# Kernel optimization log

Measured on AMD Instinct MI355X. Metric: run time of the kernel, lower is better.

## Reference

```python
import jax, jax.numpy as jnp
import numpy as np

EMBED_DIM = 1024
NUM_HEADS = 16
HEAD_DIM = EMBED_DIM // NUM_HEADS


def setup_inputs() -> dict:
    key = jax.random.key(0)
    ks = jax.random.split(key, 9)
    B, S, E = 2, 2048, EMBED_DIM
    scale = 1.0 / np.sqrt(E)
    x = jax.random.normal(ks[0], (B, S, E), dtype=jnp.float32)
    Wq = jax.random.normal(ks[1], (E, E), dtype=jnp.float32) * scale
    bq = jax.random.normal(ks[2], (E,), dtype=jnp.float32) * 0.01
    Wk = jax.random.normal(ks[3], (E, E), dtype=jnp.float32) * scale
    bk = jax.random.normal(ks[4], (E,), dtype=jnp.float32) * 0.01
    Wv = jax.random.normal(ks[5], (E, E), dtype=jnp.float32) * scale
    bv = jax.random.normal(ks[6], (E,), dtype=jnp.float32) * 0.01
    Wo = jax.random.normal(ks[7], (E, E), dtype=jnp.float32) * scale
    bo = jax.random.normal(ks[8], (E,), dtype=jnp.float32) * 0.01
    return {"x": x, "Wq": Wq, "bq": bq, "Wk": Wk, "bk": bk,
            "Wv": Wv, "bv": bv, "Wo": Wo, "bo": bo}


def reference(x, Wq, bq, Wk, bk, Wv, bv, Wo, bo):
    B, S, E = x.shape
    H, D = NUM_HEADS, HEAD_DIM
    # projections (torch Linear: x @ W.T + b), reshape to (B, H, S, D)
    q = (x @ Wq.T + bq).reshape(B, S, H, D).transpose(0, 2, 1, 3)
    k = (x @ Wk.T + bk).reshape(B, S, H, D).transpose(0, 2, 1, 3)
    v = (x @ Wv.T + bv).reshape(B, S, H, D).transpose(0, 2, 1, 3)
    softmax_scale = 1.0 / np.sqrt(D)
    # (B, H, S, S) scores, causal mask, stable softmax
    scores = softmax_scale * jnp.einsum('bhsd,bhtd->bhst', q, k)
    causal = jnp.tril(jnp.ones((S, S), dtype=bool))  # True = keep
    scores = jnp.where(causal, scores, -jnp.inf)
    attn = jax.nn.softmax(scores, axis=-1)
    out = jnp.einsum('bhst,bhtd->bhsd', attn, v)  # (B, H, S, D)
    out = out.transpose(0, 2, 1, 3).reshape(B, S, E)
    return out @ Wo.T + bo
```

## Files before the change

### kernel.cpp

```cpp
#include <hip/hip_runtime.h>
#include <cstdint>
#include <cstddef>

#define SEQ   2048
#define BATCH 2
#define EMB   1024
#define NH    16
#define HD    64
#define MTOT  (BATCH * SEQ)
#define NX    (MTOT * EMB)
#define NW    (EMB * EMB)

typedef __bf16 bf16_t;
typedef __bf16 bf16x4 __attribute__((ext_vector_type(4)));
typedef __bf16 bf16x8 __attribute__((ext_vector_type(8)));
typedef float  f32x4  __attribute__((ext_vector_type(4)));
typedef float  f32x16 __attribute__((ext_vector_type(16)));

typedef __attribute__((address_space(1))) const void* as1cv;
typedef __attribute__((address_space(3))) void*       as3v;

__device__ __forceinline__ void async_cp16(const void* g, void* l) {
  __builtin_amdgcn_global_load_lds((as1cv)g, (as3v)l, 16, 0, 0);
}

__device__ __forceinline__ f32x4 mfma16(bf16x8 a, bf16x8 b, f32x4 c) {
  return __builtin_amdgcn_mfma_f32_16x16x32_bf16(a, b, c, 0, 0, 0);
}
__device__ __forceinline__ f32x16 mfma32(bf16x8 a, bf16x8 b, f32x16 c) {
  return __builtin_amdgcn_mfma_f32_32x32x16_bf16(a, b, c, 0, 0, 0);
}

__global__ __launch_bounds__(256) void cvt_all(
    const float* __restrict__ x,  const float* __restrict__ wq,
    const float* __restrict__ wk, const float* __restrict__ wv,
    const float* __restrict__ wo,
    bf16_t* __restrict__ xb,  bf16_t* __restrict__ wqb,
    bf16_t* __restrict__ wkb, bf16_t* __restrict__ wvb,
    bf16_t* __restrict__ wob) {
  long e = ((long)blockIdx.x * 256 + threadIdx.x) * 4;
  const float* s; bf16_t* d; long off;
  if (e < NX) { s = x; d = xb; off = e; }
  else {
    long e2 = e - NX;
    int w = (int)(e2 >> 20);
    off = e2 & (NW - 1);
    s = (w == 0) ? wq : (w == 1) ? wk : (w == 2) ? wv : wo;
    d = (w == 0) ? wqb : (w == 1) ? wkb : (w == 2) ? wvb : wob;
  }
  float4 v = *(const float4*)(s + off);
  bf16x4 o;
  o[0] = (bf16_t)v.x; o[1] = (bf16_t)v.y; o[2] = (bf16_t)v.z; o[3] = (bf16_t)v.w;
  *(bf16x4*)(d + off) = o;
}

__global__ __launch_bounds__(256) void vtrans(const bf16_t* __restrict__ V,
                                              bf16_t* __restrict__ VT) {
  const int hb = blockIdx.x;
  const int sb = blockIdx.y;
  const int h = hb & 15, b = hb >> 4;
  const int t = threadIdx.x;
  __shared__ __align__(16) bf16_t Ts[64 * 72];
  const bf16_t* Vp = V + ((size_t)(b * SEQ + sb * 64)) * EMB + h * HD;
  const int sr = t >> 4, d0 = (t & 15) * 4;
#pragma unroll
  for (int i = 0; i < 4; ++i) {
    bf16x4 v = *(const bf16x4*)(Vp + (size_t)(sr + 16 * i) * EMB + d0);
    *(bf16x4*)&Ts[(sr + 16 * i) * 72 + d0] = v;
  }
  __syncthreads();
  const int d = t >> 2, tc = (t & 3) * 16;
  __align__(16) bf16_t out[16];
#pragma unroll
  for (int j = 0; j < 16; ++j) out[j] = Ts[(tc + j) * 72 + d];
  bf16_t* dst = VT + ((size_t)hb * HD + d) * SEQ + sb * 64 + tc;
  *(uint4*)(dst)     = *(uint4*)&out[0];
  *(uint4*)(dst + 8) = *(uint4*)&out[8];
}

template <typename OT>
__global__ __launch_bounds__(256) void gemm_bt3(
    const bf16_t* __restrict__ A,
    const bf16_t* __restrict__ W0, const bf16_t* __restrict__ W1,
    const bf16_t* __restrict__ W2,
    const float* __restrict__ b0, const float* __restrict__ b1,
    const float* __restrict__ b2,
    OT* __restrict__ C0, OT* __restrict__ C1, OT* __restrict__ C2) {
  constexpr int K = EMB, N = EMB, BK = 64;
  const int z = blockIdx.z;
  const bf16_t* B    = (z == 0) ? W0 : (z == 1) ? W1 : W2;
  const float*  bias = (z == 0) ? b0 : (z == 1) ? b1 : b2;
  OT*           C    = (z == 0) ? C0 : (z == 1) ? C1 : C2;

  __shared__ __align__(16) bf16_t As[128 * BK];
  __shared__ __align__(16) bf16_t Bs[128 * BK];

  const int tid  = threadIdx.x;
  const int lane = tid & 63;
  const int wave = tid >> 6;
  const int quad = lane >> 4;
  const int l16  = lane & 15;
  const int wm   = (wave >> 1) * 64;
  const int wn   = (wave & 1) * 64;
  const int m0   = blockIdx.y * 128;
  const int n0   = blockIdx.x * 128;

  const int row0 = tid >> 3;
  const int slot = tid & 7;
  const bf16_t* gA[4];
  const bf16_t* gB[4];
#pragma unroll
  for (int i = 0; i < 4; ++i) {
    const int r    = row0 + 32 * i;
    const int scol = (slot ^ (r & 7)) * 8;
    gA[i] = A + (size_t)(m0 + r) * K + scol;
    gB[i] = B + (size_t)(n0 + r) * K + scol;
  }

  f32x4 acc[4][4] = {};
  const int sw = l16 & 7;

  for (int kk = 0; kk < K; kk += BK) {
#pragma unroll
    for (int i = 0; i < 4; ++i) {
      async_cp16(gA[i] + kk, &As[(tid + 256 * i) * 8]);
      async_cp16(gB[i] + kk, &Bs[(tid + 256 * i) * 8]);
    }
    __syncthreads();

    bf16x8 af[2][4], bfr[2][4];
#pragma unroll
    for (int ks = 0; ks < 2; ++ks) {
      const int cg = ks * 4 + quad;
      const int js = (cg ^ sw) * 8;
#pragma unroll
      for (int i = 0; i < 4; ++i) {
        af[ks][i]  = *(const bf16x8*)&As[(wm + i * 16 + l16) * BK + js];
        bfr[ks][i] = *(const bf16x8*)&Bs[(wn + i * 16 + l16) * BK + js];
      }
    }
#pragma unroll
    for (int ks = 0; ks < 2; ++ks)
#pragma unroll
      for (int i = 0; i < 4; ++i)
#pragma unroll
        for (int j = 0; j < 4; ++j)
          acc[i][j] = mfma16(af[ks][i], bfr[ks][j], acc[i][j]);
    __syncthreads();
  }

#pragma unroll
  for (int j = 0; j < 4; ++j) {
    const int col = n0 + wn + j * 16 + l16;
    const float bv = bias[col];
#pragma unroll
    for (int i = 0; i < 4; ++i) {
      const int row = m0 + wm + i * 16 + quad * 4;
#pragma unroll
      for (int r = 0; r < 4; ++r) {
        C[(size_t)(row + r) * N + col] = (OT)(acc[i][j][r] + bv);
      }
    }
  }
}

__global__ __launch_bounds__(256) void attn128(
    const bf16_t* __restrict__ Qg, const bf16_t* __restrict__ Kg,
    const bf16_t* __restrict__ VTg, bf16_t* __restrict__ Og) {
  const int hb  = blockIdx.x;
  const int y   = blockIdx.y;
  const int s   = (y < 8) ? (15 - y) : (y - 8);
  const int h   = hb & 15, b = hb >> 4;
  const int tid = threadIdx.x;
  const int lane = tid & 63, wave = tid >> 6;
  const int l31 = lane & 31, hi = lane >> 5;

  __shared__ __align__(16) bf16_t Ks[2][64 * 72];
  __shared__ __align__(16) bf16_t VsT[2][64 * 72];
  __shared__ __align__(16) bf16_t PQ[128 * 72];

  const size_t base = ((size_t)b * SEQ) * EMB + (size_t)h * HD;
  const bf16_t* Kp  = Kg + base;
  const bf16_t* VTp = VTg + (size_t)hb * HD * SEQ;

  const int kr0r = tid >> 3, kcol = (tid & 7) * 8;
  const int kr1r = kr0r + 32;
  const int lo0 = (tid >> 3) * 72 + kcol;
  const int lo1 = lo0 + 32 * 72;

  bf16_t* Pw = &PQ[wave * (32 * 72)];

  const int q0  = s * 128;
  const int nit = 2 * s + 2;
  const bf16_t* Qp = Qg + base + (size_t)q0 * EMB;

  uint4 kr0 = *(const uint4*)(Kp + (size_t)kr0r * EMB + kcol);
  uint4 kr1 = *(const uint4*)(Kp + (size_t)kr1r * EMB + kcol);
  uint4 vr0 = *(const uint4*)(VTp + (size_t)kr0r * SEQ + kcol);
  uint4 vr1 = *(const uint4*)(VTp + (size_t)kr1r * SEQ + kcol);

#pragma unroll
  for (int i = 0; i < 4; ++i) {
    const int c = tid + 256 * i;
    *(uint4*)&PQ[(c >> 3) * 72 + (c & 7) * 8] =
        *(const uint4*)(Qp + (size_t)(c >> 3) * EMB + (c & 7) * 8);
  }
  __syncthreads();

  bf16x8 qf[4];
#pragma unroll
  for (int kk = 0; kk < 4; ++kk)
    qf[kk] = *(const bf16x8*)&PQ[(32 * wave + l31) * 72 + kk * 16 + hi * 8];

  f32x16 acc_o0 = {}, acc_o1 = {};
  float l_i[16];
#pragma unroll
  for (int r = 0; r < 16; ++r) l_i[r] = 0.f;

  for (int it = 0; it < nit; ++it) {
    bf16_t* Kc = &Ks[it & 1][0];
    bf16_t* Vc = &VsT[it & 1][0];
    *(uint4*)&Kc[lo0] = kr0;
    *(uint4*)&Kc[lo1] = kr1;
    *(uint4*)&Vc[lo0] = vr0;
    *(uint4*)&Vc[lo1] = vr1;
    __syncthreads();

    if (it + 1 < nit) {
      const bf16_t* Kn  = Kp + (size_t)(it + 1) * 64 * EMB;
      const bf16_t* VTn = VTp + (it + 1) * 64;
      kr0 = *(const uint4*)(Kn + (size_t)kr0r * EMB + kcol);
      kr1 = *(const uint4*)(Kn + (size_t)kr1r * EMB + kcol);
      vr0 = *(const uint4*)(VTn + (size_t)kr0r * SEQ + kcol);
      vr1 = *(const uint4*)(VTn + (size_t)kr1r * SEQ + kcol);
    }

    const bool active = (64 * it <= q0 + 32 * wave + 31);
    if (active) {
      f32x16 acc0 = {}, acc1 = {};
#pragma unroll
      for (int kk = 0; kk < 4; ++kk) {
        const bf16x8 kf0 = *(const bf16x8*)&Kc[l31 * 72 + kk * 16 + hi * 8];
        const bf16x8 kf1 =
            *(const bf16x8*)&Kc[(32 + l31) * 72 + kk * 16 + hi * 8];
        acc0 = mfma32(qf[kk], kf0, acc0);
        acc1 = mfma32(qf[kk], kf1, acc1);
      }

      constexpr float SC2 = 0.18033688011112042f;
      if (it >= nit - 2) {
        const int row0 = q0 + 32 * wave + 4 * hi;
        const int c0 = 64 * it + l31, c1 = c0 + 32;
#pragma unroll
        for (int r = 0; r < 16; ++r) {
          const int row = row0 + (r & 3) + 8 * (r >> 2);
          float p0 = exp2f(__builtin_fmaf(acc0[r], SC2, -8.f));
          float p1 = exp2f(__builtin_fmaf(acc1[r], SC2, -8.f));
          if (c0 > row) p0 = 0.f;
          if (c1 > row) p1 = 0.f;
          l_i[r] += p0 + p1;
          const int rl = (r & 3) + 8 * (r >> 2) + 4 * hi;
          Pw[rl * 72 + l31]      = (bf16_t)p0;
          Pw[rl * 72 + 32 + l31] = (bf16_t)p1;
        }
      } else {
#pragma unroll
        for (int r = 0; r < 16; ++r) {
          const float p0 = exp2f(__builtin_fmaf(acc0[r], SC2, -8.f));
          const float p1 = exp2f(__builtin_fmaf(acc1[r], SC2, -8.f));
          l_i[r] += p0 + p1;
          const int rl = (r & 3) + 8 * (r >> 2) + 4 * hi;
          Pw[rl * 72 + l31]      = (bf16_t)p0;
          Pw[rl * 72 + 32 + l31] = (bf16_t)p1;
        }
      }

#pragma unroll
      for (int kk = 0; kk < 4; ++kk) {
        const bf16x8 pf = *(const bf16x8*)&Pw[l31 * 72 + kk * 16 + hi * 8];
        const bf16x8 vf0 = *(const bf16x8*)&Vc[l31 * 72 + kk * 16 + hi * 8];
        const bf16x8 vf1 =
            *(const bf16x8*)&Vc[(32 + l31) * 72 + kk * 16 + hi * 8];
        acc_o0 = mfma32(pf, vf0, acc_o0);
        acc_o1 = mfma32(pf, vf1, acc_o1);
      }
    }
  }

  bf16_t* Op = Og + base + (size_t)(q0 + 32 * wave) * EMB;
#pragma unroll
  for (int r = 0; r < 16; ++r) {
    float rs = l_i[r];
#pragma unroll
    for (int off = 1; off < 32; off <<= 1) rs += __shfl_xor(rs, off, 64);
    const float inv = 1.f / rs;
    const int rl = (r & 3) + 8 * (r >> 2) + 4 * hi;
    Op[(size_t)rl * EMB + l31]      = (bf16_t)(acc_o0[r] * inv);
    Op[(size_t)rl * EMB + 32 + l31] = (bf16_t)(acc_o1[r] * inv);
  }
}

extern "C" void kernel_launch(void* const* d_in, const int* in_sizes, int n_in,
                              void* d_out, int out_size, void* d_ws,
                              size_t ws_size, hipStream_t stream) {
  const float* x  = (const float*)d_in[0];
  const float* Wq = (const float*)d_in[1];
  const float* bq = (const float*)d_in[2];
  const float* Wk = (const float*)d_in[3];
  const float* bk = (const float*)d_in[4];
  const float* Wv = (const float*)d_in[5];
  const float* bv = (const float*)d_in[6];
  const float* Wo = (const float*)d_in[7];
  const float* bo = (const float*)d_in[8];
  float* out = (float*)d_out;

  char* p = (char*)d_ws;
  bf16_t* xb  = (bf16_t*)p; p += (size_t)NX * 2;
  bf16_t* wqb = (bf16_t*)p; p += (size_t)NW * 2;
  bf16_t* wkb = (bf16_t*)p; p += (size_t)NW * 2;
  bf16_t* wvb = (bf16_t*)p; p += (size_t)NW * 2;
  bf16_t* wob = (bf16_t*)p; p += (size_t)NW * 2;
  bf16_t* qb  = (bf16_t*)p; p += (size_t)NX * 2;
  bf16_t* kb  = (bf16_t*)p; p += (size_t)NX * 2;
  bf16_t* vb  = (bf16_t*)p; p += (size_t)NX * 2;
  bf16_t* ab  = (bf16_t*)p; p += (size_t)NX * 2;
  bf16_t* vtb = xb;

  const int ntot = NX + 4 * NW;
  cvt_all<<<dim3(ntot / 4 / 256), 256, 0, stream>>>(
      x, Wq, Wk, Wv, Wo, xb, wqb, wkb, wvb, wob);

  gemm_bt3<bf16_t><<<dim3(EMB / 128, MTOT / 128, 3), 256, 0, stream>>>(
      xb, wqb, wkb, wvb, bq, bk, bv, qb, kb, vb);

  vtrans<<<dim3(BATCH * NH, SEQ / 64), 256, 0, stream>>>(vb, vtb);

  attn128<<<dim3(BATCH * NH, SEQ / 128), 256, 0, stream>>>(qb, kb, vtb, ab);

  gemm_bt3<float><<<dim3(EMB / 128, MTOT / 128, 1), 256, 0, stream>>>(
      ab, wob, wob, wob, bo, bo, bo, out, out, out);
}
```

Baseline: 215.0 us.

## Keep attention probabilities in registers via transposed MFMA and shrink GEMM tile

The attention kernel now computes transposed scores (K·Qᵀ) so each lane holds one query row's probabilities. The P operand for the PV matmul is built in registers with cross-half shuffles instead of a round trip through shared memory, and the per-row sum needs a single shuffle. Output is staged through LDS for coalesced 16-byte stores, and launch bounds request 3 blocks per CU. The projection GEMMs switch from 128x128 to 128x64 tiles, doubling the grid for better CU fill at the cost of less operand reuse per block.

```diff
diff --git a/kernel.cpp b/kernel.cpp
--- a/kernel.cpp
+++ b/kernel.cpp
@@ -12,6 +12,7 @@
 #define NW    (EMB * EMB)
 
 typedef __bf16 bf16_t;
+typedef __bf16 bf16x2 __attribute__((ext_vector_type(2)));
 typedef __bf16 bf16x4 __attribute__((ext_vector_type(4)));
 typedef __bf16 bf16x8 __attribute__((ext_vector_type(8)));
 typedef float  f32x4  __attribute__((ext_vector_type(4)));
@@ -29,6 +30,16 @@
 }
 __device__ __forceinline__ f32x16 mfma32(bf16x8 a, bf16x8 b, f32x16 c) {
   return __builtin_amdgcn_mfma_f32_32x32x16_bf16(a, b, c, 0, 0, 0);
+}
+
+__device__ __forceinline__ uint32_t pk2(float a, float b) {
+  bf16x2 t; t[0] = (bf16_t)a; t[1] = (bf16_t)b;
+  return __builtin_bit_cast(uint32_t, t);
+}
+__device__ __forceinline__ bf16x8 mk_frag(uint32_t x, uint32_t y,
+                                          uint32_t z, uint32_t w) {
+  uint4 u; u.x = x; u.y = y; u.z = z; u.w = w;
+  return __builtin_bit_cast(bf16x8, u);
 }
 
 __global__ __launch_bounds__(256) void cvt_all(
@@ -93,56 +104,59 @@
   OT*           C    = (z == 0) ? C0 : (z == 1) ? C1 : C2;
 
   __shared__ __align__(16) bf16_t As[128 * BK];
-  __shared__ __align__(16) bf16_t Bs[128 * BK];
+  __shared__ __align__(16) bf16_t Bs[64 * BK];
 
   const int tid  = threadIdx.x;
   const int lane = tid & 63;
   const int wave = tid >> 6;
   const int quad = lane >> 4;
   const int l16  = lane & 15;
-  const int wm   = (wave >> 1) * 64;
-  const int wn   = (wave & 1) * 64;
+  const int wm   = wave * 32;
   const int m0   = blockIdx.y * 128;
-  const int n0   = blockIdx.x * 128;
+  const int n0   = blockIdx.x * 64;
 
   const int row0 = tid >> 3;
   const int slot = tid & 7;
   const bf16_t* gA[4];
-  const bf16_t* gB[4];
+  const bf16_t* gB[2];
 #pragma unroll
   for (int i = 0; i < 4; ++i) {
-    const int r    = row0 + 32 * i;
-    const int scol = (slot ^ (r & 7)) * 8;
-    gA[i] = A + (size_t)(m0 + r) * K + scol;
-    gB[i] = B + (size_t)(n0 + r) * K + scol;
-  }
-
-  f32x4 acc[4][4] = {};
+    const int r = row0 + 32 * i;
+    gA[i] = A + (size_t)(m0 + r) * K + (slot ^ (r & 7)) * 8;
+  }
+#pragma unroll
+  for (int i = 0; i < 2; ++i) {
+    const int r = row0 + 32 * i;
+    gB[i] = B + (size_t)(n0 + r) * K + (slot ^ (r & 7)) * 8;
+  }
+
+  f32x4 acc[2][4] = {};
   const int sw = l16 & 7;
 
   for (int kk = 0; kk < K; kk += BK) {
 #pragma unroll
-    for (int i = 0; i < 4; ++i) {
+    for (int i = 0; i < 4; ++i)
       async_cp16(gA[i] + kk, &As[(tid + 256 * i) * 8]);
+#pragma unroll
+    for (int i = 0; i < 2; ++i)
       async_cp16(gB[i] + kk, &Bs[(tid + 256 * i) * 8]);
-    }
     __syncthreads();
 
-    bf16x8 af[2][4], bfr[2][4];
+    bf16x8 af[2][2], bfr[2][4];
 #pragma unroll
     for (int ks = 0; ks < 2; ++ks) {
-      const int cg = ks * 4 + quad;
-      const int js = (cg ^ sw) * 8;
-#pragma unroll
-      for (int i = 0; i < 4; ++i) {
-        af[ks][i]  = *(const bf16x8*)&As[(wm + i * 16 + l16) * BK + js];
-        bfr[ks][i] = *(const bf16x8*)&Bs[(wn + i * 16 + l16) * BK + js];
-      }
+      const int js = ((ks * 4 + quad) ^ sw) * 8;
+#pragma unroll
+      for (int i = 0; i < 2; ++i)
+        af[ks][i] = *(const bf16x8*)&As[(wm + i * 16 + l16) * BK + js];
+#pragma unroll
+      for (int j = 0; j < 4; ++j)
+        bfr[ks][j] = *(const bf16x8*)&Bs[(j * 16 + l16) * BK + js];
     }
 #pragma unroll
     for (int ks = 0; ks < 2; ++ks)
 #pragma unroll
-      for (int i = 0; i < 4; ++i)
+      for (int i = 0; i < 2; ++i)
 #pragma unroll
         for (int j = 0; j < 4; ++j)
           acc[i][j] = mfma16(af[ks][i], bfr[ks][j], acc[i][j]);
@@ -151,10 +165,10 @@
 
 #pragma unroll
   for (int j = 0; j < 4; ++j) {
-    const int col = n0 + wn + j * 16 + l16;
+    const int col = n0 + j * 16 + l16;
     const float bv = bias[col];
 #pragma unroll
-    for (int i = 0; i < 4; ++i) {
+    for (int i = 0; i < 2; ++i) {
       const int row = m0 + wm + i * 16 + quad * 4;
 #pragma unroll
       for (int r = 0; r < 4; ++r) {
@@ -164,7 +178,7 @@
   }
 }
 
-__global__ __launch_bounds__(256) void attn128(
+__global__ __launch_bounds__(256, 3) void attn128(
     const bf16_t* __restrict__ Qg, const bf16_t* __restrict__ Kg,
     const bf16_t* __restrict__ VTg, bf16_t* __restrict__ Og) {
   const int hb  = blockIdx.x;
@@ -174,10 +188,11 @@
   const int tid = threadIdx.x;
   const int lane = tid & 63, wave = tid >> 6;
   const int l31 = lane & 31, hi = lane >> 5;
+  const bool h0 = (hi == 0);
 
   __shared__ __align__(16) bf16_t Ks[2][64 * 72];
   __shared__ __align__(16) bf16_t VsT[2][64 * 72];
-  __shared__ __align__(16) bf16_t PQ[128 * 72];
+  __shared__ __align__(16) bf16_t Qs[128 * 64];
 
   const size_t base = ((size_t)b * SEQ) * EMB + (size_t)h * HD;
   const bf16_t* Kp  = Kg + base;
@@ -185,10 +200,8 @@
 
   const int kr0r = tid >> 3, kcol = (tid & 7) * 8;
   const int kr1r = kr0r + 32;
-  const int lo0 = (tid >> 3) * 72 + kcol;
+  const int lo0 = kr0r * 72 + kcol;
   const int lo1 = lo0 + 32 * 72;
-
-  bf16_t* Pw = &PQ[wave * (32 * 72)];
 
   const int q0  = s * 128;
   const int nit = 2 * s + 2;
@@ -202,7 +215,7 @@
 #pragma unroll
   for (int i = 0; i < 4; ++i) {
     const int c = tid + 256 * i;
-    *(uint4*)&PQ[(c >> 3) * 72 + (c & 7) * 8] =
+    *(uint4*)&Qs[(c >> 3) * 64 + (c & 7) * 8] =
         *(const uint4*)(Qp + (size_t)(c >> 3) * EMB + (c & 7) * 8);
   }
   __syncthreads();
@@ -210,12 +223,10 @@
   bf16x8 qf[4];
 #pragma unroll
   for (int kk = 0; kk < 4; ++kk)
-    qf[kk] = *(const bf16x8*)&PQ[(32 * wave + l31) * 72 + kk * 16 + hi * 8];
-
-  f32x16 acc_o0 = {}, acc_o1 = {};
-  float l_i[16];
-#pragma unroll
-  for (int r = 0; r < 16; ++r) l_i[r] = 0.f;
+    qf[kk] = *(const bf16x8*)&Qs[(32 * wave + l31) * 64 + kk * 16 + hi * 8];
+
+  f32x16 acc_t0 = {}, acc_t1 = {};
+  float lsum = 0.f;
 
   for (int it = 0; it < nit; ++it) {
     bf16_t* Kc = &Ks[it & 1][0];
@@ -237,66 +248,89 @@
 
     const bool active = (64 * it <= q0 + 32 * wave + 31);
     if (active) {
-      f32x16 acc0 = {}, acc1 = {};
+      f32x16 s0 = {}, s1 = {};
 #pragma unroll
       for (int kk = 0; kk < 4; ++kk) {
         const bf16x8 kf0 = *(const bf16x8*)&Kc[l31 * 72 + kk * 16 + hi * 8];
         const bf16x8 kf1 =
             *(const bf16x8*)&Kc[(32 + l31) * 72 + kk * 16 + hi * 8];
-        acc0 = mfma32(qf[kk], kf0, acc0);
-        acc1 = mfma32(qf[kk], kf1, acc1);
+        s0 = mfma32(kf0, qf[kk], s0);
+        s1 = mfma32(kf1, qf[kk], s1);
       }
 
       constexpr float SC2 = 0.18033688011112042f;
       if (it >= nit - 2) {
-        const int row0 = q0 + 32 * wave + 4 * hi;
-        const int c0 = 64 * it + l31, c1 = c0 + 32;
+        const int qg = q0 + 32 * wave + l31;
+        const int k0 = 64 * it + 4 * hi;
 #pragma unroll
         for (int r = 0; r < 16; ++r) {
-          const int row = row0 + (r & 3) + 8 * (r >> 2);
-          float p0 = exp2f(__builtin_fmaf(acc0[r], SC2, -8.f));
-          float p1 = exp2f(__builtin_fmaf(acc1[r], SC2, -8.f));
-          if (c0 > row) p0 = 0.f;
-          if (c1 > row) p1 = 0.f;
-          l_i[r] += p0 + p1;
-          const int rl = (r & 3) + 8 * (r >> 2) + 4 * hi;
-          Pw[rl * 72 + l31]      = (bf16_t)p0;
-          Pw[rl * 72 + 32 + l31] = (bf16_t)p1;
+          const int key = k0 + (r & 3) + 8 * (r >> 2);
+          float p0 = exp2f(__builtin_fmaf(s0[r], SC2, -8.f));
+          float p1 = exp2f(__builtin_fmaf(s1[r], SC2, -8.f));
+          if (key > qg) p0 = 0.f;
+          if (key + 32 > qg) p1 = 0.f;
+          s0[r] = p0; s1[r] = p1;
+          lsum += p0 + p1;
         }
       } else {
 #pragma unroll
         for (int r = 0; r < 16; ++r) {
-          const float p0 = exp2f(__builtin_fmaf(acc0[r], SC2, -8.f));
-          const float p1 = exp2f(__builtin_fmaf(acc1[r], SC2, -8.f));
-          l_i[r] += p0 + p1;
-          const int rl = (r & 3) + 8 * (r >> 2) + 4 * hi;
-          Pw[rl * 72 + l31]      = (bf16_t)p0;
-          Pw[rl * 72 + 32 + l31] = (bf16_t)p1;
+          const float p0 = exp2f(__builtin_fmaf(s0[r], SC2, -8.f));
+          const float p1 = exp2f(__builtin_fmaf(s1[r], SC2, -8.f));
+          s0[r] = p0; s1[r] = p1;
+          lsum += p0 + p1;
         }
       }
 
+      bf16x8 pf[4];
 #pragma unroll
       for (int kk = 0; kk < 4; ++kk) {
-        const bf16x8 pf = *(const bf16x8*)&Pw[l31 * 72 + kk * 16 + hi * 8];
+        const f32x16& g = (kk < 2) ? s0 : s1;
+        const int bir = 8 * (kk & 1);
+        const uint32_t PL0 = pk2(g[bir + 0], g[bir + 1]);
+        const uint32_t PL1 = pk2(g[bir + 2], g[bir + 3]);
+        const uint32_t PH0 = pk2(g[bir + 4], g[bir + 5]);
+        const uint32_t PH1 = pk2(g[bir + 6], g[bir + 7]);
+        const uint32_t XL0 = (uint32_t)__shfl_xor((int)PL0, 32, 64);
+        const uint32_t XL1 = (uint32_t)__shfl_xor((int)PL1, 32, 64);
+        const uint32_t XH0 = (uint32_t)__shfl_xor((int)PH0, 32, 64);
+        const uint32_t XH1 = (uint32_t)__shfl_xor((int)PH1, 32, 64);
+        pf[kk] = h0 ? mk_frag(PL0, PL1, XL0, XL1)
+                    : mk_frag(XH0, XH1, PH0, PH1);
+      }
+
+#pragma unroll
+      for (int kk = 0; kk < 4; ++kk) {
         const bf16x8 vf0 = *(const bf16x8*)&Vc[l31 * 72 + kk * 16 + hi * 8];
         const bf16x8 vf1 =
             *(const bf16x8*)&Vc[(32 + l31) * 72 + kk * 16 + hi * 8];
-        acc_o0 = mfma32(pf, vf0, acc_o0);
-        acc_o1 = mfma32(pf, vf1, acc_o1);
-      }
-    }
-  }
-
+        acc_t0 = mfma32(vf0, pf[kk], acc_t0);
+        acc_t1 = mfma32(vf1, pf[kk], acc_t1);
+      }
+    }
+  }
+
+  const float lt = lsum + __shfl_xor(lsum, 32, 64);
+  const float inv = 1.f / lt;
+  bf16_t* Ow = &Qs[(32 * wave) * 64];
+#pragma unroll
+  for (int a = 0; a < 4; ++a)
+#pragma unroll
+    for (int c = 0; c < 4; c += 2) {
+      const int r = 4 * a + c;
+      const int d = c + 8 * a + 4 * hi;
+      *(uint32_t*)&Ow[l31 * 64 + d] =
+          pk2(acc_t0[r] * inv, acc_t0[r + 1] * inv);
+      *(uint32_t*)&Ow[l31 * 64 + d + 32] =
+          pk2(acc_t1[r] * inv, acc_t1[r + 1] * inv);
+    }
   bf16_t* Op = Og + base + (size_t)(q0 + 32 * wave) * EMB;
 #pragma unroll
-  for (int r = 0; r < 16; ++r) {
-    float rs = l_i[r];
-#pragma unroll
-    for (int off = 1; off < 32; off <<= 1) rs += __shfl_xor(rs, off, 64);
-    const float inv = 1.f / rs;
-    const int rl = (r & 3) + 8 * (r >> 2) + 4 * hi;
-    Op[(size_t)rl * EMB + l31]      = (bf16_t)(acc_o0[r] * inv);
-    Op[(size_t)rl * EMB + 32 + l31] = (bf16_t)(acc_o1[r] * inv);
+  for (int i = 0; i < 4; ++i) {
+    const int id = lane + 64 * i;
+    const int row = id >> 3, col8 = (id & 7) * 8;
+    *(uint4*)(Op + (size_t)row * EMB + col8) =
+        *(const uint4*)&Ow[row * 64 + col8];
   }
 }
 
@@ -330,13 +364,13 @@
   cvt_all<<<dim3(ntot / 4 / 256), 256, 0, stream>>>(
       x, Wq, Wk, Wv, Wo, xb, wqb, wkb, wvb, wob);
 
-  gemm_bt3<bf16_t><<<dim3(EMB / 128, MTOT / 128, 3), 256, 0, stream>>>(
+  gemm_bt3<bf16_t><<<dim3(EMB / 64, MTOT / 128, 3), 256, 0, stream>>>(
       xb, wqb, wkb, wvb, bq, bk, bv, qb, kb, vb);
 
   vtrans<<<dim3(BATCH * NH, SEQ / 64), 256, 0, stream>>>(vb, vtb);
 
   attn128<<<dim3(BATCH * NH, SEQ / 128), 256, 0, stream>>>(qb, kb, vtb, ab);
 
-  gemm_bt3<float><<<dim3(EMB / 128, MTOT / 128, 1), 256, 0, stream>>>(
+  gemm_bt3<float><<<dim3(EMB / 64, MTOT / 128, 1), 256, 0, stream>>>(
       ab, wob, wob, wob, bo, bo, bo, out, out, out);
 }
```

Result: faster. 191.6 us (-10.8%).
